# Performance work log

Measured on AMD Instinct MI355X. Metric: run time of the kernel, lower is better.

## Reference

```python
import jax, jax.numpy as jnp
import numpy as np

T, B, V, D, H, C = 2048, 32, 50257, 512, 768, 10


def setup_inputs() -> dict:
    key = jax.random.key(0)
    ks = jax.random.split(key, 11)
    s = 0.02
    return {
        "x": jax.random.randint(ks[0], (T, B), 0, V),
        "embed_table": jax.random.normal(ks[1], (V, D), jnp.float32) * s,
        "W_x": jax.random.normal(ks[2], (H, D), jnp.float32) * s,
        "W_f": jax.random.normal(ks[3], (H, D), jnp.float32) * s,
        "b_f": jax.random.normal(ks[4], (H,), jnp.float32) * s,
        "W_r": jax.random.normal(ks[5], (H, D), jnp.float32) * s,
        "b_r": jax.random.normal(ks[6], (H,), jnp.float32) * s,
        "W_cx": jax.random.normal(ks[7], (H, D), jnp.float32) * s,
        "b_cx": jax.random.normal(ks[8], (H,), jnp.float32) * s,
        "W_out": jax.random.normal(ks[9], (C, H), jnp.float32) * s,
        "b_out": jax.random.normal(ks[10], (C,), jnp.float32) * s,
    }


def reference(x, embed_table, W_x, W_f, b_f, W_r, b_r, W_cx, b_cx, W_out, b_out):
    # Embedding lookup: [T, B, D]
    e = embed_table[x]
    # Precompute all gate projections for every timestep (batched GEMMs).
    xp = jnp.einsum("tbd,hd->tbh", e, W_x)                 # x_t projection
    f = jax.nn.sigmoid(jnp.einsum("tbd,hd->tbh", e, W_f) + b_f)   # forget gate
    r = jax.nn.sigmoid(jnp.einsum("tbd,hd->tbh", e, W_r) + b_r)   # reset gate
    cx = jnp.einsum("tbd,hd->tbh", e, W_cx) + b_cx                # highway path

    c0 = jnp.zeros((B, H), e.dtype)  # init_hidden: zeros

    def step(c, inp):
        f_t, xp_t, r_t, cx_t = inp
        c = f_t * c + (1.0 - f_t) * xp_t
        h = r_t * jnp.tanh(c) + (1.0 - r_t) * cx_t
        return c, h

    _, ht = jax.lax.scan(step, c0, (f, xp, r, cx))  # ht: [T, B, H]

    # tanh -> max-pool over time -> tanh -> classifier
    pooled = jnp.max(jnp.tanh(ht), axis=0)          # [B, H]
    pooled = jnp.tanh(pooled)
    logit = pooled @ W_out.T + b_out                # [B, C]
    return logit
```

## Files before the change

kernel.cpp:

```cpp
#include <hip/hip_runtime.h>
#include <hip/hip_bf16.h>
#include <cstdint>
#include <cstddef>

#define T_DIM 2048
#define B_DIM 32
#define D_DIM 512
#define H_DIM 768
#define C_DIM 10
#define K_DIM D_DIM
#define N_DIM (4 * H_DIM)

#define TC 1024
#define NCHUNK (T_DIM / TC)
#define MC (TC * B_DIM)

#define L_SEG 32
#define S_SEG (TC / L_SEG)
#define BH (B_DIM * H_DIM)

typedef __attribute__((ext_vector_type(8))) short short8;
typedef __attribute__((ext_vector_type(4))) float float4v;

__device__ inline unsigned short f2bf(float f) {
  unsigned int u = __builtin_bit_cast(unsigned int, f);
  unsigned int r = (u + 0x7FFFu + ((u >> 16) & 1u)) >> 16;
  return (unsigned short)r;
}
__device__ inline float bf2f(unsigned short s) {
  unsigned int u = ((unsigned int)s) << 16;
  return __builtin_bit_cast(float, u);
}
__device__ inline float fast_rcp(float x) { return __builtin_amdgcn_rcpf(x); }
__device__ inline float fast_exp2(float x) { return __builtin_amdgcn_exp2f(x); }
__device__ inline float sigmoid_f(float x) {
  float e = fast_exp2(-1.4426950408889634f * x);
  return fast_rcp(1.0f + e);
}
__device__ inline float tanh_f(float x) {
  float e = fast_exp2(2.885390081777927f * x);
  return 1.0f - 2.0f * fast_rcp(e + 1.0f);
}
__device__ inline void gld16(const unsigned short* g, unsigned short* l) {
  __builtin_amdgcn_global_load_lds(
      (const __attribute__((address_space(1))) void*)g,
      (__attribute__((address_space(3))) void*)l, 16, 0, 0);
}
__device__ inline unsigned int pack_bf16x2(float lo, float hi) {
  return ((unsigned int)f2bf(hi) << 16) | (unsigned int)f2bf(lo);
}

__global__ __launch_bounds__(256) void gather_embed_kernel(
    const int* __restrict__ x_c, const float* __restrict__ table,
    unsigned short* __restrict__ ebfc) {
  int idx = blockIdx.x * 256 + threadIdx.x;
  int m = idx >> 7;
  int k4 = (idx & 127) << 2;
  int row = x_c[m];
  float4 v = *(const float4*)(table + (size_t)row * D_DIM + k4);
  ushort4 o;
  o.x = f2bf(v.x); o.y = f2bf(v.y); o.z = f2bf(v.z); o.w = f2bf(v.w);
  *(ushort4*)(ebfc + (size_t)m * D_DIM + k4) = o;
}

__global__ __launch_bounds__(256) void convert_w_kernel(
    const float* __restrict__ Wx, const float* __restrict__ Wf,
    const float* __restrict__ Wr, const float* __restrict__ Wcx,
    unsigned short* __restrict__ wcat) {
  int idx = blockIdx.x * 256 + threadIdx.x;
  int n = idx >> 7;
  int k4 = (idx & 127) << 2;
  int mat = n / H_DIM;
  int h = n - mat * H_DIM;
  const float* src = (mat == 0) ? Wx : (mat == 1) ? Wf : (mat == 2) ? Wr : Wcx;
  float4 v = *(const float4*)(src + (size_t)h * D_DIM + k4);
  ushort4 o;
  o.x = f2bf(v.x); o.y = f2bf(v.y); o.z = f2bf(v.z); o.w = f2bf(v.w);
  *(ushort4*)(wcat + (size_t)n * D_DIM + k4) = o;
}

#define BMT 128
#define BNT 256
#define BKT 32
#define NT (K_DIM / BKT)
#define BUF_SH 12288

__device__ __forceinline__ float4v mfma16(short8 a, short8 b, float4v c) {
  return __builtin_amdgcn_mfma_f32_16x16x32_bf16(a, b, c, 0, 0, 0);
}

__device__ __forceinline__ void stgA(const unsigned short* srcA, unsigned short* sm,
                                     int buf, int kt, int tid) {
  const unsigned short* s = srcA + kt * BKT;
  unsigned short* d = sm + buf * BUF_SH + tid * 8;
  gld16(s, d);
  gld16(s + (size_t)128 * K_DIM, d + 4096);
}
__device__ __forceinline__ void stgB(const unsigned short* srcB, unsigned short* sm,
                                     int buf, int kt, int tid) {
  gld16(srcB + kt * BKT, sm + buf * BUF_SH + 8192 + tid * 8);
}

template <int STG, int VMN>
__device__ __forceinline__ void tile_step(
    int u, unsigned short* sm, const unsigned short* srcA,
    const unsigned short* srcB, int tid, int aO, int bO,
    float4v (&acc)[4][4]) {
  unsigned short* c = sm + (u % 3) * BUF_SH;
  const int sbuf = (u + 2) % 3;
  short8 a[4], b[4];
#pragma unroll
  for (int f = 0; f < 4; f++) a[f] = *(const short8*)(c + aO + f * 512);
  b[0] = *(const short8*)(c + bO);
  b[1] = *(const short8*)(c + bO + 512);
  if constexpr (STG) stgA(srcA, sm, sbuf, u + 2, tid);
  __builtin_amdgcn_sched_barrier(0);
  __builtin_amdgcn_s_barrier();
  __builtin_amdgcn_s_setprio(1);
#pragma unroll
  for (int f = 0; f < 4; f++) {
    acc[f][0] = mfma16(a[f], b[0], acc[f][0]);
    acc[f][1] = mfma16(a[f], b[1], acc[f][1]);
  }
  __builtin_amdgcn_s_setprio(0);
  __builtin_amdgcn_sched_barrier(0);
  b[2] = *(const short8*)(c + bO + 1024);
  b[3] = *(const short8*)(c + bO + 1536);
  if constexpr (STG) stgB(srcB, sm, sbuf, u + 2, tid);
  __builtin_amdgcn_sched_barrier(0);
  __builtin_amdgcn_s_setprio(1);
#pragma unroll
  for (int f = 0; f < 4; f++) {
    acc[f][2] = mfma16(a[f], b[2], acc[f][2]);
    acc[f][3] = mfma16(a[f], b[3], acc[f][3]);
  }
  __builtin_amdgcn_s_setprio(0);
  __builtin_amdgcn_sched_barrier(0);
  if constexpr (VMN == 3)
    asm volatile("s_waitcnt vmcnt(3)" ::: "memory");
  else if constexpr (VMN == 0)
    asm volatile("s_waitcnt vmcnt(0)" ::: "memory");
  __builtin_amdgcn_s_barrier();
}

__global__ __launch_bounds__(512, 4) void gemm_kernel(
    const unsigned short* __restrict__ ebfc,
    const unsigned short* __restrict__ wcat,
    const float* __restrict__ b_f, const float* __restrict__ b_r,
    const float* __restrict__ b_cx,
    unsigned short* __restrict__ projc) {
  __shared__ __align__(16) unsigned short smem[36864];

  const int tid = threadIdx.x;
  const int wave = tid >> 6;
  const int lane = tid & 63;
  const int quad = lane >> 4;
  const int l16 = lane & 15;
  const int wn = wave >> 1;
  const int wm = wave & 1;

  const int orig = blockIdx.x;
  const int swz = (orig & 7) * 384 + (orig >> 3);
  const int n_idx = swz % 12;
  const int m_idx = swz / 12;
  const int n0 = n_idx * BNT;
  const int m0 = m_idx * BMT;

  const int arow = tid >> 2;
  const int kchx = (tid & 3) ^ ((arow >> 1) & 3);
  const unsigned short* srcA = wcat + (size_t)(n0 + arow) * K_DIM + kchx * 8;
  const unsigned short* srcB = ebfc + (size_t)(m0 + arow) * K_DIM + kchx * 8;

  const int xr = (quad ^ ((l16 >> 1) & 3)) * 8;
  const int aO = (wn * 64 + l16) * 32 + xr;
  const int bO = 8192 + (wm * 64 + l16) * 32 + xr;

  float4v acc[4][4] = {};

  stgA(srcA, smem, 0, 0, tid);
  stgB(srcB, smem, 0, 0, tid);
  stgA(srcA, smem, 1, 1, tid);
  stgB(srcB, smem, 1, 1, tid);
  asm volatile("s_waitcnt vmcnt(3)" ::: "memory");
  __builtin_amdgcn_s_barrier();

#pragma unroll
  for (int u = 0; u < NT - 2; u++)
    tile_step<1, 3>(u, smem, srcA, srcB, tid, aO, bO, acc);
  tile_step<0, 0>(NT - 2, smem, srcA, srcB, tid, aO, bO, acc);
  tile_step<0, -1>(NT - 1, smem, srcA, srcB, tid, aO, bO, acc);

  __syncthreads();
  int mat = n0 / H_DIM;
  int hb = n0 - mat * H_DIM;
  size_t matBase = (size_t)mat * MC * H_DIM;
  const float* bias = (mat == 1) ? b_f : (mat == 2) ? b_r : b_cx;
#pragma unroll
  for (int f = 0; f < 4; f++) {
    int hl = wn * 64 + f * 16 + quad * 4;
    float4 bv;
    if (mat == 0) { bv.x = bv.y = bv.z = bv.w = 0.0f; }
    else          { bv = *(const float4*)(bias + hb + hl); }
#pragma unroll
    for (int g = 0; g < 4; g++) {
      int ml = wm * 64 + g * 16 + l16;
      float v0 = acc[f][g][0] + bv.x;
      float v1 = acc[f][g][1] + bv.y;
      float v2 = acc[f][g][2] + bv.z;
      float v3 = acc[f][g][3] + bv.w;
      if (mat == 1 || mat == 2) {
        v0 = sigmoid_f(v0); v1 = sigmoid_f(v1);
        v2 = sigmoid_f(v2); v3 = sigmoid_f(v3);
      }
      uint2 pk;
      pk.x = pack_bf16x2(v0, v1);
      pk.y = pack_bf16x2(v2, v3);
      int log8 = hl >> 2;
      int phys8 = log8 ^ ((ml & 7) << 1);
      *(uint2*)(smem + ml * 256 + phys8 * 4) = pk;
    }
  }
  __syncthreads();
#pragma unroll
  for (int it = 0; it < 8; it++) {
    int idx = it * 512 + tid;
    int ml = idx >> 5;
    int c16 = idx & 31;
    int phys16 = c16 ^ (ml & 7);
    short8 v = *(const short8*)(smem + ml * 256 + phys16 * 8);
    *(short8*)(projc + matBase + (size_t)(m0 + ml) * H_DIM + hb + c16 * 8) = v;
  }
}

__global__ __launch_bounds__(512) void scan_fused_kernel(
    const unsigned short* __restrict__ projc,
    float* __restrict__ c_state, float* __restrict__ hm,
    float* __restrict__ pooled, int first) {
  __shared__ float4 Pl[S_SEG][16];
  __shared__ float4 Ql[S_SEG][16];
  const int tid = threadIdx.x;
  const int seg = tid >> 4;
  const int slot = tid & 15;
  const int q = blockIdx.x;
  const int e4 = q * 64 + slot * 4;
  const size_t mstr = (size_t)MC * H_DIM;
  const size_t idx0 = (size_t)(seg * L_SEG) * BH + e4;

  float p0 = 1.f, p1 = 1.f, p2 = 1.f, p3 = 1.f;
  float q0 = 0.f, q1 = 0.f, q2 = 0.f, q3 = 0.f;
#pragma unroll 4
  for (int t = 0; t < L_SEG; t++) {
    size_t id = idx0 + (size_t)t * BH;
    ushort4 xp = *(const ushort4*)(projc + id);
    ushort4 ff = *(const ushort4*)(projc + mstr + id);
    float f0 = bf2f(ff.x), f1 = bf2f(ff.y), f2 = bf2f(ff.z), f3 = bf2f(ff.w);
    q0 = fmaf(f0, q0 - bf2f(xp.x), bf2f(xp.x));
    q1 = fmaf(f1, q1 - bf2f(xp.y), bf2f(xp.y));
    q2 = fmaf(f2, q2 - bf2f(xp.z), bf2f(xp.z));
    q3 = fmaf(f3, q3 - bf2f(xp.w), bf2f(xp.w));
    p0 *= f0; p1 *= f1; p2 *= f2; p3 *= f3;
  }
  Pl[seg][slot] = make_float4(p0, p1, p2, p3);
  Ql[seg][slot] = make_float4(q0, q1, q2, q3);
  __syncthreads();

  if (tid < 64) {
    int sl = tid >> 2, el = tid & 3;
    int ge = q * 64 + sl * 4 + el;
    float c = first ? 0.f : c_state[ge];
#pragma unroll 4
    for (int s = 0; s < S_SEG; s++) {
      float* Pp = (float*)&Pl[s][sl];
      const float* Qp = (const float*)&Ql[s][sl];
      float P = Pp[el], Q = Qp[el];
      Pp[el] = c;
      c = fmaf(P, c, Q);
    }
    c_state[ge] = c;
  }
  __syncthreads();

  float4 cv = Pl[seg][slot];
  float c0 = cv.x, c1 = cv.y, c2 = cv.z, c3 = cv.w;
  float m0 = -1e30f, m1 = -1e30f, m2 = -1e30f, m3 = -1e30f;
#pragma unroll 2
  for (int t = 0; t < L_SEG; t++) {
    size_t id = idx0 + (size_t)t * BH;
    ushort4 xp = *(const ushort4*)(projc + id);
    ushort4 ff = *(const ushort4*)(projc + mstr + id);
    ushort4 rr = *(const ushort4*)(projc + 2 * mstr + id);
    ushort4 cx = *(const ushort4*)(projc + 3 * mstr + id);
    c0 = fmaf(bf2f(ff.x), c0 - bf2f(xp.x), bf2f(xp.x));
    c1 = fmaf(bf2f(ff.y), c1 - bf2f(xp.y), bf2f(xp.y));
    c2 = fmaf(bf2f(ff.z), c2 - bf2f(xp.z), bf2f(xp.z));
    c3 = fmaf(bf2f(ff.w), c3 - bf2f(xp.w), bf2f(xp.w));
    float h0 = fmaf(bf2f(rr.x), tanh_f(c0) - bf2f(cx.x), bf2f(cx.x));
    float h1 = fmaf(bf2f(rr.y), tanh_f(c1) - bf2f(cx.y), bf2f(cx.y));
    float h2 = fmaf(bf2f(rr.z), tanh_f(c2) - bf2f(cx.z), bf2f(cx.z));
    float h3 = fmaf(bf2f(rr.w), tanh_f(c3) - bf2f(cx.w), bf2f(cx.w));
    m0 = fmaxf(m0, h0); m1 = fmaxf(m1, h1);
    m2 = fmaxf(m2, h2); m3 = fmaxf(m3, h3);
  }
  __syncthreads();
  Ql[seg][slot] = make_float4(m0, m1, m2, m3);
  __syncthreads();

  if (tid < 64) {
    int sl = tid >> 2, el = tid & 3;
    int ge = q * 64 + sl * 4 + el;
    float mm = -1e30f;
#pragma unroll 4
    for (int s = 0; s < S_SEG; s++) mm = fmaxf(mm, ((const float*)&Ql[s][sl])[el]);
    if (first) hm[ge] = mm;
    else       pooled[ge] = tanh_f(tanh_f(fmaxf(hm[ge], mm)));
  }
}

__global__ __launch_bounds__(64) void classifier_kernel(
    const float* __restrict__ pooled, const float* __restrict__ W_out,
    const float* __restrict__ b_out, float* __restrict__ out) {
  int b = blockIdx.x / C_DIM;
  int c = blockIdx.x % C_DIM;
  int lane = threadIdx.x;
  float s = 0.0f;
#pragma unroll
  for (int i = 0; i < H_DIM / 64; i++) {
    int h = i * 64 + lane;
    s += pooled[(size_t)b * H_DIM + h] * W_out[(size_t)c * H_DIM + h];
  }
#pragma unroll
  for (int off = 32; off; off >>= 1) s += __shfl_down(s, off, 64);
  if (lane == 0) out[b * C_DIM + c] = s + b_out[c];
}

extern "C" void kernel_launch(void* const* d_in, const int* in_sizes, int n_in,
                              void* d_out, int out_size, void* d_ws, size_t ws_size,
                              hipStream_t stream) {
  const int*   x     = (const int*)d_in[0];
  const float* table = (const float*)d_in[1];
  const float* W_x   = (const float*)d_in[2];
  const float* W_f   = (const float*)d_in[3];
  const float* b_f   = (const float*)d_in[4];
  const float* W_r   = (const float*)d_in[5];
  const float* b_r   = (const float*)d_in[6];
  const float* W_cx  = (const float*)d_in[7];
  const float* b_cx  = (const float*)d_in[8];
  const float* W_out = (const float*)d_in[9];
  const float* b_out = (const float*)d_in[10];

  char* ws = (char*)d_ws;
  size_t off = 0;
  unsigned short* wcat  = (unsigned short*)(ws + off); off += (size_t)N_DIM * K_DIM * 2;
  unsigned short* ebfc  = (unsigned short*)(ws + off); off += (size_t)MC * K_DIM * 2;
  unsigned short* projc = (unsigned short*)(ws + off); off += (size_t)4 * MC * H_DIM * 2;
  float* c_st   = (float*)(ws + off); off += (size_t)BH * 4;
  float* hm     = (float*)(ws + off); off += (size_t)BH * 4;
  float* pooled = (float*)(ws + off); off += (size_t)BH * 4;

  convert_w_kernel<<<(N_DIM * K_DIM / 4) / 256, 256, 0, stream>>>(W_x, W_f, W_r, W_cx, wcat);

  for (int ch = 0; ch < NCHUNK; ch++) {
    gather_embed_kernel<<<(MC * K_DIM / 4) / 256, 256, 0, stream>>>(x + (size_t)ch * MC, table, ebfc);
    gemm_kernel<<<(N_DIM / BNT) * (MC / BMT), 512, 0, stream>>>(ebfc, wcat, b_f, b_r, b_cx, projc);
    scan_fused_kernel<<<BH / 64, 512, 0, stream>>>(projc, c_st, hm, pooled, ch == 0);
  }
  classifier_kernel<<<B_DIM * C_DIM, 64, 0, stream>>>(pooled, W_out, b_out, (float*)d_out);
}
```

Baseline: 525.6 us.

## Interleave gate projections per row and widen scan loads to 8 bf16

The GEMM epilogue now writes the four gate outputs interleaved per (t,b) row as [m][4][H] instead of four separate planes. The scan kernel reads all four gates from adjacent addresses with 16-byte short8 loads covering 8 hidden units per thread. It also moves to 256-thread blocks indexed by (batch, 64-hidden slice). The goal is better locality and fewer, wider memory transactions in the bandwidth-bound scan, at the cost of more registers per thread.

```diff
diff --git a/kernel.cpp b/kernel.cpp
--- a/kernel.cpp
+++ b/kernel.cpp
@@ -193,7 +193,6 @@
   __syncthreads();
   int mat = n0 / H_DIM;
   int hb = n0 - mat * H_DIM;
-  size_t matBase = (size_t)mat * MC * H_DIM;
   const float* bias = (mat == 1) ? b_f : (mat == 2) ? b_r : b_cx;
 #pragma unroll
   for (int f = 0; f < 4; f++) {
@@ -228,89 +227,93 @@
     int c16 = idx & 31;
     int phys16 = c16 ^ (ml & 7);
     short8 v = *(const short8*)(smem + ml * 256 + phys16 * 8);
-    *(short8*)(projc + matBase + (size_t)(m0 + ml) * H_DIM + hb + c16 * 8) = v;
-  }
-}
-
-__global__ __launch_bounds__(512) void scan_fused_kernel(
+    *(short8*)(projc + ((size_t)(m0 + ml) * 4 + mat) * H_DIM + hb + c16 * 8) = v;
+  }
+}
+
+__global__ __launch_bounds__(256) void scan_fused_kernel(
     const unsigned short* __restrict__ projc,
     float* __restrict__ c_state, float* __restrict__ hm,
     float* __restrict__ pooled, int first) {
-  __shared__ float4 Pl[S_SEG][16];
-  __shared__ float4 Ql[S_SEG][16];
+  __shared__ float Pl[S_SEG][64];
+  __shared__ float Ql[S_SEG][64];
   const int tid = threadIdx.x;
-  const int seg = tid >> 4;
-  const int slot = tid & 15;
+  const int seg = tid >> 3;
+  const int slot = tid & 7;
   const int q = blockIdx.x;
-  const int e4 = q * 64 + slot * 4;
-  const size_t mstr = (size_t)MC * H_DIM;
-  const size_t idx0 = (size_t)(seg * L_SEG) * BH + e4;
-
-  float p0 = 1.f, p1 = 1.f, p2 = 1.f, p3 = 1.f;
-  float q0 = 0.f, q1 = 0.f, q2 = 0.f, q3 = 0.f;
+  const int b = q / 12;
+  const int h0 = (q % 12) * 64 + slot * 8;
+  const size_t tstr = (size_t)B_DIM * 4 * H_DIM;
+  const size_t base = ((size_t)(seg * L_SEG) * B_DIM + b) * 4 * H_DIM + h0;
+
+  float p[8], qv[8];
+#pragma unroll
+  for (int i = 0; i < 8; i++) { p[i] = 1.f; qv[i] = 0.f; }
+  size_t ad = base;
 #pragma unroll 4
   for (int t = 0; t < L_SEG; t++) {
-    size_t id = idx0 + (size_t)t * BH;
-    ushort4 xp = *(const ushort4*)(projc + id);
-    ushort4 ff = *(const ushort4*)(projc + mstr + id);
-    float f0 = bf2f(ff.x), f1 = bf2f(ff.y), f2 = bf2f(ff.z), f3 = bf2f(ff.w);
-    q0 = fmaf(f0, q0 - bf2f(xp.x), bf2f(xp.x));
-    q1 = fmaf(f1, q1 - bf2f(xp.y), bf2f(xp.y));
-    q2 = fmaf(f2, q2 - bf2f(xp.z), bf2f(xp.z));
-    q3 = fmaf(f3, q3 - bf2f(xp.w), bf2f(xp.w));
-    p0 *= f0; p1 *= f1; p2 *= f2; p3 *= f3;
-  }
-  Pl[seg][slot] = make_float4(p0, p1, p2, p3);
-  Ql[seg][slot] = make_float4(q0, q1, q2, q3);
+    short8 xp = *(const short8*)(projc + ad);
+    short8 ff = *(const short8*)(projc + ad + H_DIM);
+#pragma unroll
+    for (int i = 0; i < 8; i++) {
+      float fi = bf2f((unsigned short)ff[i]);
+      float xi = bf2f((unsigned short)xp[i]);
+      qv[i] = fmaf(fi, qv[i] - xi, xi);
+      p[i] *= fi;
+    }
+    ad += tstr;
+  }
+  *(float4*)&Pl[seg][slot * 8]     = make_float4(p[0], p[1], p[2], p[3]);
+  *(float4*)&Pl[seg][slot * 8 + 4] = make_float4(p[4], p[5], p[6], p[7]);
+  *(float4*)&Ql[seg][slot * 8]     = make_float4(qv[0], qv[1], qv[2], qv[3]);
+  *(float4*)&Ql[seg][slot * 8 + 4] = make_float4(qv[4], qv[5], qv[6], qv[7]);
   __syncthreads();
 
   if (tid < 64) {
-    int sl = tid >> 2, el = tid & 3;
-    int ge = q * 64 + sl * 4 + el;
+    int ge = q * 64 + tid;
     float c = first ? 0.f : c_state[ge];
 #pragma unroll 4
     for (int s = 0; s < S_SEG; s++) {
-      float* Pp = (float*)&Pl[s][sl];
-      const float* Qp = (const float*)&Ql[s][sl];
-      float P = Pp[el], Q = Qp[el];
-      Pp[el] = c;
+      float P = Pl[s][tid], Q = Ql[s][tid];
+      Pl[s][tid] = c;
       c = fmaf(P, c, Q);
     }
     c_state[ge] = c;
   }
   __syncthreads();
 
-  float4 cv = Pl[seg][slot];
-  float c0 = cv.x, c1 = cv.y, c2 = cv.z, c3 = cv.w;
-  float m0 = -1e30f, m1 = -1e30f, m2 = -1e30f, m3 = -1e30f;
+  float c[8], mx[8];
+#pragma unroll
+  for (int i = 0; i < 8; i++) { c[i] = Pl[seg][slot * 8 + i]; mx[i] = -1e30f; }
+  ad = base;
 #pragma unroll 2
   for (int t = 0; t < L_SEG; t++) {
-    size_t id = idx0 + (size_t)t * BH;
-    ushort4 xp = *(const ushort4*)(projc + id);
-    ushort4 ff = *(const ushort4*)(projc + mstr + id);
-    ushort4 rr = *(const ushort4*)(projc + 2 * mstr + id);
-    ushort4 cx = *(const ushort4*)(projc + 3 * mstr + id);
-    c0 = fmaf(bf2f(ff.x), c0 - bf2f(xp.x), bf2f(xp.x));
-    c1 = fmaf(bf2f(ff.y), c1 - bf2f(xp.y), bf2f(xp.y));
-    c2 = fmaf(bf2f(ff.z), c2 - bf2f(xp.z), bf2f(xp.z));
-    c3 = fmaf(bf2f(ff.w), c3 - bf2f(xp.w), bf2f(xp.w));
-    float h0 = fmaf(bf2f(rr.x), tanh_f(c0) - bf2f(cx.x), bf2f(cx.x));
-    float h1 = fmaf(bf2f(rr.y), tanh_f(c1) - bf2f(cx.y), bf2f(cx.y));
-    float h2 = fmaf(bf2f(rr.z), tanh_f(c2) - bf2f(cx.z), bf2f(cx.z));
-    float h3 = fmaf(bf2f(rr.w), tanh_f(c3) - bf2f(cx.w), bf2f(cx.w));
-    m0 = fmaxf(m0, h0); m1 = fmaxf(m1, h1);
-    m2 = fmaxf(m2, h2); m3 = fmaxf(m3, h3);
-  }
-  __syncthreads();
-  Ql[seg][slot] = make_float4(m0, m1, m2, m3);
+    short8 xp = *(const short8*)(projc + ad);
+    short8 ff = *(const short8*)(projc + ad + H_DIM);
+    short8 rr = *(const short8*)(projc + ad + 2 * H_DIM);
+    short8 cx = *(const short8*)(projc + ad + 3 * H_DIM);
+#pragma unroll
+    for (int i = 0; i < 8; i++) {
+      float fi = bf2f((unsigned short)ff[i]);
+      float xi = bf2f((unsigned short)xp[i]);
+      float ri = bf2f((unsigned short)rr[i]);
+      float ci = bf2f((unsigned short)cx[i]);
+      c[i] = fmaf(fi, c[i] - xi, xi);
+      float h = fmaf(ri, tanh_f(c[i]) - ci, ci);
+      mx[i] = fmaxf(mx[i], h);
+    }
+    ad += tstr;
+  }
+  __syncthreads();
+  *(float4*)&Ql[seg][slot * 8]     = make_float4(mx[0], mx[1], mx[2], mx[3]);
+  *(float4*)&Ql[seg][slot * 8 + 4] = make_float4(mx[4], mx[5], mx[6], mx[7]);
   __syncthreads();
 
   if (tid < 64) {
-    int sl = tid >> 2, el = tid & 3;
-    int ge = q * 64 + sl * 4 + el;
+    int ge = q * 64 + tid;
     float mm = -1e30f;
 #pragma unroll 4
-    for (int s = 0; s < S_SEG; s++) mm = fmaxf(mm, ((const float*)&Ql[s][sl])[el]);
+    for (int s = 0; s < S_SEG; s++) mm = fmaxf(mm, Ql[s][tid]);
     if (first) hm[ge] = mm;
     else       pooled[ge] = tanh_f(tanh_f(fmaxf(hm[ge], mm)));
   }
@@ -362,7 +365,7 @@
   for (int ch = 0; ch < NCHUNK; ch++) {
     gather_embed_kernel<<<(MC * K_DIM / 4) / 256, 256, 0, stream>>>(x + (size_t)ch * MC, table, ebfc);
     gemm_kernel<<<(N_DIM / BNT) * (MC / BMT), 512, 0, stream>>>(ebfc, wcat, b_f, b_r, b_cx, projc);
-    scan_fused_kernel<<<BH / 64, 512, 0, stream>>>(projc, c_st, hm, pooled, ch == 0);
+    scan_fused_kernel<<<BH / 64, 256, 0, stream>>>(projc, c_st, hm, pooled, ch == 0);
   }
   classifier_kernel<<<B_DIM * C_DIM, 64, 0, stream>>>(pooled, W_out, b_out, (float*)d_out);
 }
```

Measured after the change: 519.3 us. About the same (-1.2%).
